# Optimization experiments

Hardware: AMD Instinct MI355X
Metric: run time of the kernel (lower is better)

The kernel has to match this reference:

```python
import jax, jax.numpy as jnp
import numpy as np
from jax import lax

B, D = 512, 256
C = 10  # hidden conv channels


def setup_inputs() -> dict:
    key = jax.random.key(0)
    ks = jax.random.split(key, 9)
    x = jax.random.normal(ks[0], (B, D, D), jnp.float32)
    w1 = jax.random.normal(ks[1], (C, 1, 1, 1), jnp.float32) * 0.1   # Conv2d(1,10,1)
    b1 = jax.random.normal(ks[2], (C,), jnp.float32) * 0.01
    w2 = jax.random.normal(ks[3], (1, C, 3, 3), jnp.float32) * 0.05  # Conv2d(10,1,3,1,1)
    b2 = jax.random.normal(ks[4], (1,), jnp.float32) * 0.01
    fc1_w = jax.random.normal(ks[5], (4, D * B), jnp.float32) * (1.0 / np.sqrt(D * B))
    fc1_b = jax.random.normal(ks[6], (4,), jnp.float32) * 0.01
    fc2_w = jax.random.normal(ks[7], (2, 4), jnp.float32) * 0.5
    fc2_b = jax.random.normal(ks[8], (2,), jnp.float32) * 0.01
    return {"x": x, "w1": w1, "b1": b1, "w2": w2, "b2": b2,
            "fc1_w": fc1_w, "fc1_b": fc1_b, "fc2_w": fc2_w, "fc2_b": fc2_b}


def reference(x, w1, b1, w2, b2, fc1_w, fc1_b, fc2_w, fc2_b):
    # edge-to-edge: E[b,i,j] = row_sum(i) + col_sum(j)
    rs = x.sum(axis=-1)          # [B, D]
    cs = x.sum(axis=-2)          # [B, D]
    e = (rs[:, :, None] + cs[:, None, :])[:, None]  # [B, 1, D, D]
    # Conv2d(1, C, 1) == per-pixel scale+bias over channels
    h = jax.nn.relu(e * w1.reshape(1, C, 1, 1) + b1.reshape(1, C, 1, 1))  # [B, C, D, D]
    # convSym: lower-triangular mask each channel
    h = h * jnp.tril(jnp.ones((D, D), jnp.float32))
    # Conv2d(C, 1, 3, stride=1, pad=1)
    y = lax.conv_general_dilated(h, w2, (1, 1), 'SAME',
                                 dimension_numbers=('NCHW', 'OIHW', 'NCHW'))
    y = jax.nn.relu(y + b2.reshape(1, 1, 1, 1))[:, 0]  # [B, D, D]
    # edge-to-vertex: v[b,i] = row_sum + col_sum
    v = y.sum(axis=-1) + y.sum(axis=-2)  # [B, D]
    flat = v.reshape(-1)                  # [B*D]
    hfc = jax.nn.relu(fc1_w @ flat + fc1_b)
    return fc2_w @ hfc + fc2_b            # [2]
```

## Files before the change

### kernel.cpp

```cpp
#include <hip/hip_runtime.h>

#define DD 256
#define BB 512
#define NL 2048

#define OFF_RS   0
#define OFF_CSP  131072
#define OFF_HFC  655360
#define OFF_PAR  655368
#define OFF_TABP 655376
#define OFF_LUT  655648

typedef float v2f __attribute__((ext_vector_type(2)));

__device__ __forceinline__ v2f mk2(float a, float b) { v2f r; r.x = a; r.y = b; return r; }

__device__ __forceinline__ v2f fma2(v2f a, v2f b, v2f c) {
#if __has_builtin(__builtin_elementwise_fma)
  return __builtin_elementwise_fma(a, b, c);
#else
  return mk2(fmaf(a.x, b.x, c.x), fmaf(a.y, b.y, c.y));
#endif
}

__device__ __forceinline__ float wave_red(float v) {
#pragma unroll
  for (int off = 32; off > 0; off >>= 1) v += __shfl_down(v, off, 64);
  return v;
}

__global__ __launch_bounds__(256) void sum_kernel(const float* __restrict__ x,
                                                  const float* __restrict__ w1,
                                                  const float* __restrict__ b1,
                                                  const float* __restrict__ w2,
                                                  float* __restrict__ ws) {
  const int bq = blockIdx.x;
  const int tid = threadIdx.x;
  if (bq == 2048) {
    const int t = tid;
    float w1v[10], b1v[10], bp[10];
    int rank[10];
#pragma unroll
    for (int c = 0; c < 10; ++c) { w1v[c] = w1[c]; b1v[c] = b1[c]; bp[c] = -b1v[c] / w1v[c]; }
#pragma unroll
    for (int c = 0; c < 10; ++c) {
      int r = 0;
#pragma unroll
      for (int k = 0; k < 10; ++k)
        r += (bp[k] < bp[c] || (bp[k] == bp[c] && k < c)) ? 1 : 0;
      rank[c] = r;
    }
    float lo = bp[0], hi = bp[0];
#pragma unroll
    for (int c = 1; c < 10; ++c) { lo = fminf(lo, bp[c]); hi = fmaxf(hi, bp[c]); }
    const float step = (hi - lo) / (float)(NL - 3);
    if (t == 0) {
      ws[OFF_PAR]     = (float)(NL - 3) / (hi - lo);
      ws[OFF_PAR + 1] = 1.0f - lo * ((float)(NL - 3) / (hi - lo));
    }
    if (t < 99) {
      const int s = t / 9, tt = t % 9;
      const int dr = tt / 3, kc = tt % 3;
      float A = 0.f, Bv = 0.f;
      for (int c = 0; c < 10; ++c) {
        bool act = (w1v[c] > 0.f) ? (rank[c] < s)
                 : ((w1v[c] < 0.f) ? (rank[c] >= s) : (b1v[c] > 0.f));
        if (act) { A += w1v[c] * w2[c * 9 + tt]; Bv += b1v[c] * w2[c * 9 + tt]; }
      }
      const int base = (s * 3 + kc) * 8;
      const int posA = (dr == 2) ? 4 : dr;
      const int posB = (dr == 2) ? 5 : (2 + dr);
      ws[OFF_TABP + base + posA] = A;
      ws[OFF_TABP + base + posB] = Bv;
      ws[OFF_TABP + base + 6] = 0.f;
      ws[OFF_TABP + base + 7] = 0.f;
    }
    unsigned short* lut = (unsigned short*)(ws + OFF_LUT);
    for (int k = t; k < NL; k += 256) {
      const float xx = lo + (float)(k - 1) * step;
      int s = 0;
#pragma unroll
      for (int c = 0; c < 10; ++c) s += (bp[c] < xx) ? 1 : 0;
      lut[k] = (unsigned short)(s * 96);
    }
    return;
  }
  const int b = bq >> 2;
  const int q = bq & 3;
  const int lane = tid & 63;
  const int wv = tid >> 6;
  __shared__ float rowp[64][65];
  __shared__ float csl[4][DD];
  __shared__ float segp[4][64];
  float4 cacc = make_float4(0.f, 0.f, 0.f, 0.f);
  const float4* px = (const float4*)(x + ((size_t)b << 16) + ((size_t)(q * 64 + wv * 16) << 8));
#pragma unroll
  for (int r = 0; r < 16; ++r) {
    float4 val = px[r * 64 + lane];
    cacc.x += val.x; cacc.y += val.y; cacc.z += val.z; cacc.w += val.w;
    rowp[wv * 16 + r][lane] = (val.x + val.y) + (val.z + val.w);
  }
  ((float4*)csl[wv])[lane] = cacc;
  __syncthreads();
  {
    const int row = tid & 63, seg = tid >> 6;
    const float* rp = rowp[row] + seg * 16;
    float s = 0.f;
#pragma unroll
    for (int k = 0; k < 16; ++k) s += rp[k];
    segp[seg][row] = s;
  }
  __syncthreads();
  if (tid < 64)
    ws[OFF_RS + b * DD + q * 64 + tid] =
        (segp[0][tid] + segp[1][tid]) + (segp[2][tid] + segp[3][tid]);
  ws[OFF_CSP + bq * DD + tid] =
      (csl[0][tid] + csl[1][tid]) + (csl[2][tid] + csl[3][tid]);
  if (bq == 0 && tid < 4) ws[OFF_HFC + tid] = 0.f;
}

__global__ __launch_bounds__(1024, 8) void conv_kernel(const float* __restrict__ b2p,
                                                       const float* __restrict__ fc1w,
                                                       float* __restrict__ ws) {
  const int b = blockIdx.x;
  const int tid = threadIdx.x;
  const int w = tid >> 6;
  const int lane = tid & 63;
  const int seg = w >> 2;
  const int wb = (w - seg) & 3;
  const int j = wb * 64 + lane;
  const int jmin = wb * 64;
  const int r0 = seg * 64, r1 = r0 + 64;

  __shared__ __align__(16) float tabP[264];
  __shared__ float rs_s[DD];
  __shared__ float cs_s[DD];
  __shared__ __align__(16) float wkA[DD][4];
  __shared__ unsigned short lut_s[NL];
  __shared__ float segsum_s[4][4];
  __shared__ float red_s[64];

  ((unsigned int*)lut_s)[tid] = ((const unsigned int*)(ws + OFF_LUT))[tid];
  if (tid < 256) {
    rs_s[tid] = ws[OFF_RS + b * DD + tid];
  } else if (tid < 512) {
    const int t = tid - 256;
    const float* csp = ws + OFF_CSP + (b * 4) * DD + t;
    cs_s[t] = (csp[0] + csp[DD]) + (csp[2 * DD] + csp[3 * DD]);
  } else if (tid < 768) {
    const int r = tid - 512;
#pragma unroll
    for (int k = 0; k < 4; ++k) wkA[r][k] = fc1w[k * (BB * DD) + b * DD + r];
  } else {
    const int u = tid - 768;
    if (u < 256) tabP[u] = ws[OFF_TABP + u];
  }
  if (tid < 8) tabP[256 + tid] = ws[OFF_TABP + 256 + tid];
  __syncthreads();
  if (tid < 16) {
    const int ss = tid >> 2, k = tid & 3;
    float s = 0.f;
#pragma unroll
    for (int r = 0; r < 64; ++r) s += wkA[ss * 64 + r][k];
    segsum_s[ss][k] = s;
  }
  __syncthreads();

  const float inv_step = ws[OFF_PAR];
  const float bias = ws[OFF_PAR + 1];
  const float b2v = b2p[0];
  const float yb = fmaxf(b2v, 0.f);
  const float fxmax = (float)(NL - 1);

  float csr[3], vf[3];
  csr[0] = (j >= 1) ? cs_s[j - 1] : 0.f;
  csr[1] = cs_s[j];
  csr[2] = (j < DD - 1) ? cs_s[j + 1] : 0.f;
  vf[0] = (j >= 1) ? 1.f : 0.f;
  vf[1] = 1.f;
  vf[2] = (j < DD - 1) ? 1.f : 0.f;
  v2f vf2[3];
#pragma unroll
  for (int kc = 0; kc < 3; ++kc) vf2[kc] = mk2(vf[kc], vf[kc]);

  const int nt = min(max(jmin - 2 - r0, 0), 64);
  const int rfirst = r0 + nt;
  const int iend = (r1 == DD) ? DD - 1 : r1;

  float P = 0.f, Q = 0.f;
  float vcol = 64.f * yb;
  v2f a01 = mk2(yb * segsum_s[seg][0], yb * segsum_s[seg][1]);
  v2f a23 = mk2(yb * segsum_s[seg][2], yb * segsum_s[seg][3]);

#define TAP_CORE(KC, E, M2, MS)                                              \
  {                                                                          \
    float fx = fmaf((E), inv_step, bias);                                    \
    fx = fminf(fmaxf(fx, 0.f), fxmax);                                       \
    const int off = (int)lut_s[(int)fx];                                     \
    const char* tp = (const char*)tabP + (off + (KC) * 32);                  \
    const float4 ab = *(const float4*)tp;                   \
    const float2 ab2 = *(const float2*)(tp + 16);                 \
    v2f tv = fma2(mk2(ab.x, ab.y), mk2((E), (E)), mk2(ab.z, ab.w));          \
    R01 = fma2((M2), tv, R01);                                               \
    R2 = fmaf((MS), fmaf(ab2.x, (E), ab2.y), R2);                            \
  }

  if (rfirst < r1) {
    if (seg > wb) {
      for (int i = r0 - 1; i <= r0; ++i) {
        const float rsv = rs_s[i];
        v2f R01 = mk2(0.f, 0.f); float R2 = 0.f;
#pragma unroll
        for (int kc = 0; kc < 3; ++kc) {
          const float e = rsv + csr[kc];
          const float m = ((j - 1 + kc) <= i) ? vf[kc] : 0.f;
          TAP_CORE(kc, e, mk2(m, m), m)
        }
        P = Q + R01.y; Q = R01.x;
      }
      for (int i = r0 + 1; i <= iend; ++i) {
        const float rsv = rs_s[i];
        v2f R01 = mk2(0.f, 0.f); float R2 = 0.f;
#pragma unroll
        for (int kc = 0; kc < 3; ++kc) {
          const float e = rsv + csr[kc];
          TAP_CORE(kc, e, vf2[kc], vf[kc])
        }
        const float yd = fmaxf(P + R2 + b2v, 0.f) - yb;
        vcol += yd;
        const float4 wkv = *(const float4*)wkA[i - 1];
        a01 = fma2(mk2(yd, yd), mk2(wkv.x, wkv.y), a01);
        a23 = fma2(mk2(yd, yd), mk2(wkv.z, wkv.w), a23);
        P = Q + R01.y; Q = R01.x;
      }
    } else {
      const int ibeg = (nt > 0) ? rfirst - 1 : ((r0 == 0) ? 0 : r0 - 1);
      const int ffrom = rfirst + 1;
      for (int i = ibeg; i <= iend; ++i) {
        const float rsv = rs_s[i];
        v2f R01 = mk2(0.f, 0.f); float R2 = 0.f;
        if (j - 1 <= i) {
#pragma unroll
          for (int kc = 0; kc < 3; ++kc) {
            const float e = rsv + csr[kc];
            const float m = ((j - 1 + kc) <= i) ? vf[kc] : 0.f;
            TAP_CORE(kc, e, mk2(m, m), m)
          }
        }
        if (i >= ffrom) {
          const float yd = fmaxf(P + R2 + b2v, 0.f) - yb;
          vcol += yd;
          const float4 wkv = *(const float4*)wkA[i - 1];
          a01 = fma2(mk2(yd, yd), mk2(wkv.x, wkv.y), a01);
          a23 = fma2(mk2(yd, yd), mk2(wkv.z, wkv.w), a23);
        }
        P = Q + R01.y; Q = R01.x;
      }
    }
  }
  if (r1 == DD) {
    const float yd = fmaxf(P + b2v, 0.f) - yb;
    vcol += yd;
    const float4 wkv = *(const float4*)wkA[DD - 1];
    a01 = fma2(mk2(yd, yd), mk2(wkv.x, wkv.y), a01);
    a23 = fma2(mk2(yd, yd), mk2(wkv.z, wkv.w), a23);
  }

  const float4 wkj = *(const float4*)wkA[j];
  a01 = fma2(mk2(vcol, vcol), mk2(wkj.x, wkj.y), a01);
  a23 = fma2(mk2(vcol, vcol), mk2(wkj.z, wkj.w), a23);

  float acc0 = wave_red(a01.x), acc1 = wave_red(a01.y);
  float acc2 = wave_red(a23.x), acc3 = wave_red(a23.y);
  if (lane == 0) {
    red_s[w * 4 + 0] = acc0; red_s[w * 4 + 1] = acc1;
    red_s[w * 4 + 2] = acc2; red_s[w * 4 + 3] = acc3;
  }
  __syncthreads();
  if (tid < 4) {
    float s = 0.f;
#pragma unroll
    for (int wv = 0; wv < 16; ++wv) s += red_s[wv * 4 + tid];
    atomicAdd(&ws[OFF_HFC + tid], s);
  }
#undef TAP_CORE
}

__global__ void fc_kernel(const float* __restrict__ fc1b, const float* __restrict__ fc2w,
                          const float* __restrict__ fc2b, const float* __restrict__ ws,
                          float* __restrict__ out) {
  if (threadIdx.x == 0 && blockIdx.x == 0) {
    float o0 = fc2b[0], o1 = fc2b[1];
#pragma unroll
    for (int k = 0; k < 4; ++k) {
      float h = fmaxf(ws[OFF_HFC + k] + fc1b[k], 0.f);
      o0 += fc2w[k] * h;
      o1 += fc2w[4 + k] * h;
    }
    out[0] = o0; out[1] = o1;
  }
}

extern "C" void kernel_launch(void* const* d_in, const int* in_sizes, int n_in,
                              void* d_out, int out_size, void* d_ws, size_t ws_size,
                              hipStream_t stream) {
  const float* x    = (const float*)d_in[0];
  const float* w1   = (const float*)d_in[1];
  const float* b1   = (const float*)d_in[2];
  const float* w2   = (const float*)d_in[3];
  const float* b2   = (const float*)d_in[4];
  const float* fc1w = (const float*)d_in[5];
  const float* fc1b = (const float*)d_in[6];
  const float* fc2w = (const float*)d_in[7];
  const float* fc2b = (const float*)d_in[8];
  float* out = (float*)d_out;
  float* ws  = (float*)d_ws;

  hipLaunchKernelGGL(sum_kernel,  dim3(2049), dim3(256), 0, stream, x, w1, b1, w2, ws);
  hipLaunchKernelGGL(conv_kernel, dim3(512), dim3(1024), 0, stream, b2, fc1w, ws);
  hipLaunchKernelGGL(fc_kernel,   dim3(1), dim3(64), 0, stream, fc1b, fc2w, fc2b, ws, out);
}
```

Baseline: 241.6 us.

## Fuse sum and conv kernels into one per-batch kernel with LDS-staged loads

Merges the row/column-sum pass and the conv/FC pass into a single kernel with one block per batch. Each block streams its 256x256 slice into LDS with double-buffered global_load_lds and computes row sums via wave reductions. Each block also recomputes the breakpoint tables and LUT locally instead of reading them from a workspace. Per-block FC partials go to the workspace and a 256-thread final kernel reduces them, replacing the global atomics. This removes a launch and the workspace round-trip, but the x read now runs with only 512 blocks of 1024 threads and less parallelism per batch.

Result: slower. 255.8 us (+5.9%).

```diff
diff --git a/kernel.cpp b/kernel.cpp
--- a/kernel.cpp
+++ b/kernel.cpp
@@ -4,12 +4,7 @@
 #define BB 512
 #define NL 2048
 
-#define OFF_RS   0
-#define OFF_CSP  131072
-#define OFF_HFC  655360
-#define OFF_PAR  655368
-#define OFF_TABP 655376
-#define OFF_LUT  655648
+#define OFF_PART 0
 
 typedef float v2f __attribute__((ext_vector_type(2)));
 
@@ -29,39 +24,62 @@
   return v;
 }
 
-__global__ __launch_bounds__(256) void sum_kernel(const float* __restrict__ x,
-                                                  const float* __restrict__ w1,
-                                                  const float* __restrict__ b1,
-                                                  const float* __restrict__ w2,
-                                                  float* __restrict__ ws) {
-  const int bq = blockIdx.x;
+__device__ __forceinline__ void glds16(const float* src, float* lds_dst) {
+  __builtin_amdgcn_global_load_lds(
+      (const __attribute__((address_space(1))) unsigned int*)src,
+      (__attribute__((address_space(3))) unsigned int*)lds_dst, 16, 0, 0);
+}
+
+__global__ __launch_bounds__(1024, 4) void fused_kernel(
+    const float* __restrict__ x, const float* __restrict__ w1,
+    const float* __restrict__ b1, const float* __restrict__ w2,
+    const float* __restrict__ b2p, const float* __restrict__ fc1w,
+    float* __restrict__ ws) {
+  const int b = blockIdx.x;
   const int tid = threadIdx.x;
-  if (bq == 2048) {
-    const int t = tid;
+  const int w = tid >> 6;
+  const int lane = tid & 63;
+
+  __shared__ __align__(16) float stage[16 * 2 * DD];
+  __shared__ __align__(16) float tabP[264];
+  __shared__ float rs_s[DD];
+  __shared__ float cs_s[DD];
+  __shared__ __align__(16) float wkA[DD][4];
+  __shared__ unsigned short lut_s[NL];
+  __shared__ __align__(16) float csl[16][DD];
+  __shared__ float segsum_s[4][4];
+  __shared__ float red_s[64];
+
+  float wk0 = 0.f, wk1 = 0.f, wk2 = 0.f, wk3 = 0.f;
+  if (tid < 256) {
+    wk0 = fc1w[0 * (BB * DD) + b * DD + tid];
+    wk1 = fc1w[1 * (BB * DD) + b * DD + tid];
+    wk2 = fc1w[2 * (BB * DD) + b * DD + tid];
+    wk3 = fc1w[3 * (BB * DD) + b * DD + tid];
+  }
+
+  {
     float w1v[10], b1v[10], bp[10];
-    int rank[10];
 #pragma unroll
     for (int c = 0; c < 10; ++c) { w1v[c] = w1[c]; b1v[c] = b1[c]; bp[c] = -b1v[c] / w1v[c]; }
-#pragma unroll
-    for (int c = 0; c < 10; ++c) {
-      int r = 0;
-#pragma unroll
-      for (int k = 0; k < 10; ++k)
-        r += (bp[k] < bp[c] || (bp[k] == bp[c] && k < c)) ? 1 : 0;
-      rank[c] = r;
-    }
     float lo = bp[0], hi = bp[0];
 #pragma unroll
     for (int c = 1; c < 10; ++c) { lo = fminf(lo, bp[c]); hi = fmaxf(hi, bp[c]); }
     const float step = (hi - lo) / (float)(NL - 3);
-    if (t == 0) {
-      ws[OFF_PAR]     = (float)(NL - 3) / (hi - lo);
-      ws[OFF_PAR + 1] = 1.0f - lo * ((float)(NL - 3) / (hi - lo));
-    }
-    if (t < 99) {
-      const int s = t / 9, tt = t % 9;
+    if (tid < 99) {
+      int rank[10];
+#pragma unroll
+      for (int c = 0; c < 10; ++c) {
+        int r = 0;
+#pragma unroll
+        for (int k = 0; k < 10; ++k)
+          r += (bp[k] < bp[c] || (bp[k] == bp[c] && k < c)) ? 1 : 0;
+        rank[c] = r;
+      }
+      const int s = tid / 9, tt = tid % 9;
       const int dr = tt / 3, kc = tt % 3;
       float A = 0.f, Bv = 0.f;
+#pragma unroll
       for (int c = 0; c < 10; ++c) {
         bool act = (w1v[c] > 0.f) ? (rank[c] < s)
                  : ((w1v[c] < 0.f) ? (rank[c] >= s) : (b1v[c] > 0.f));
@@ -70,104 +88,78 @@
       const int base = (s * 3 + kc) * 8;
       const int posA = (dr == 2) ? 4 : dr;
       const int posB = (dr == 2) ? 5 : (2 + dr);
-      ws[OFF_TABP + base + posA] = A;
-      ws[OFF_TABP + base + posB] = Bv;
-      ws[OFF_TABP + base + 6] = 0.f;
-      ws[OFF_TABP + base + 7] = 0.f;
-    }
-    unsigned short* lut = (unsigned short*)(ws + OFF_LUT);
-    for (int k = t; k < NL; k += 256) {
+      tabP[base + posA] = A;
+      tabP[base + posB] = Bv;
+      tabP[base + 6] = 0.f;
+      tabP[base + 7] = 0.f;
+    }
+    for (int k = tid; k < NL; k += 1024) {
       const float xx = lo + (float)(k - 1) * step;
       int s = 0;
 #pragma unroll
       for (int c = 0; c < 10; ++c) s += (bp[c] < xx) ? 1 : 0;
-      lut[k] = (unsigned short)(s * 96);
-    }
-    return;
-  }
-  const int b = bq >> 2;
-  const int q = bq & 3;
-  const int lane = tid & 63;
-  const int wv = tid >> 6;
-  __shared__ float rowp[64][65];
-  __shared__ float csl[4][DD];
-  __shared__ float segp[4][64];
-  float4 cacc = make_float4(0.f, 0.f, 0.f, 0.f);
-  const float4* px = (const float4*)(x + ((size_t)b << 16) + ((size_t)(q * 64 + wv * 16) << 8));
-#pragma unroll
-  for (int r = 0; r < 16; ++r) {
-    float4 val = px[r * 64 + lane];
-    cacc.x += val.x; cacc.y += val.y; cacc.z += val.z; cacc.w += val.w;
-    rowp[wv * 16 + r][lane] = (val.x + val.y) + (val.z + val.w);
-  }
-  ((float4*)csl[wv])[lane] = cacc;
+      lut_s[k] = (unsigned short)(s * 96);
+    }
+  }
+
+  {
+    float* mystage = &stage[w * (2 * DD)];
+    const float* gx = x + ((size_t)b << 16) + (size_t)(w * 16) * DD;
+    glds16(gx + 0 * DD + lane * 4, mystage + 0);
+    glds16(gx + 1 * DD + lane * 4, mystage + DD);
+    float4 cacc = make_float4(0.f, 0.f, 0.f, 0.f);
+#pragma unroll
+    for (int r = 0; r < 16; ++r) {
+      if (r < 15) asm volatile("s_waitcnt vmcnt(1)" ::: "memory");
+      else        asm volatile("s_waitcnt vmcnt(0)" ::: "memory");
+      __builtin_amdgcn_sched_barrier(0);
+      const float4 v = ((const float4*)(mystage + (r & 1) * DD))[lane];
+      cacc.x += v.x; cacc.y += v.y; cacc.z += v.z; cacc.w += v.w;
+      float rsum = (v.x + v.y) + (v.z + v.w);
+      __builtin_amdgcn_sched_barrier(0);
+      if (r + 2 < 16)
+        glds16(gx + (r + 2) * DD + lane * 4, mystage + (r & 1) * DD);
+      rsum = wave_red(rsum);
+      if (lane == 0) rs_s[w * 16 + r] = rsum;
+    }
+    ((float4*)csl[w])[lane] = cacc;
+    if (tid < 256) { wkA[tid][0] = wk0; wkA[tid][1] = wk1; wkA[tid][2] = wk2; wkA[tid][3] = wk3; }
+  }
   __syncthreads();
-  {
-    const int row = tid & 63, seg = tid >> 6;
-    const float* rp = rowp[row] + seg * 16;
+  if (tid < 256) {
+    float s0 = 0.f;
+#pragma unroll
+    for (int q = 0; q < 16; ++q) s0 += csl[q][tid];
+    cs_s[tid] = s0;
+  } else if (tid < 272) {
+    const int t = tid - 256;
+    const int ss = t >> 2, k = t & 3;
     float s = 0.f;
 #pragma unroll
-    for (int k = 0; k < 16; ++k) s += rp[k];
-    segp[seg][row] = s;
+    for (int r = 0; r < 64; ++r) s += wkA[ss * 64 + r][k];
+    segsum_s[ss][k] = s;
   }
   __syncthreads();
-  if (tid < 64)
-    ws[OFF_RS + b * DD + q * 64 + tid] =
-        (segp[0][tid] + segp[1][tid]) + (segp[2][tid] + segp[3][tid]);
-  ws[OFF_CSP + bq * DD + tid] =
-      (csl[0][tid] + csl[1][tid]) + (csl[2][tid] + csl[3][tid]);
-  if (bq == 0 && tid < 4) ws[OFF_HFC + tid] = 0.f;
-}
-
-__global__ __launch_bounds__(1024, 8) void conv_kernel(const float* __restrict__ b2p,
-                                                       const float* __restrict__ fc1w,
-                                                       float* __restrict__ ws) {
-  const int b = blockIdx.x;
-  const int tid = threadIdx.x;
-  const int w = tid >> 6;
-  const int lane = tid & 63;
+
   const int seg = w >> 2;
   const int wb = (w - seg) & 3;
   const int j = wb * 64 + lane;
   const int jmin = wb * 64;
   const int r0 = seg * 64, r1 = r0 + 64;
 
-  __shared__ __align__(16) float tabP[264];
-  __shared__ float rs_s[DD];
-  __shared__ float cs_s[DD];
-  __shared__ __align__(16) float wkA[DD][4];
-  __shared__ unsigned short lut_s[NL];
-  __shared__ float segsum_s[4][4];
-  __shared__ float red_s[64];
-
-  ((unsigned int*)lut_s)[tid] = ((const unsigned int*)(ws + OFF_LUT))[tid];
-  if (tid < 256) {
-    rs_s[tid] = ws[OFF_RS + b * DD + tid];
-  } else if (tid < 512) {
-    const int t = tid - 256;
-    const float* csp = ws + OFF_CSP + (b * 4) * DD + t;
-    cs_s[t] = (csp[0] + csp[DD]) + (csp[2 * DD] + csp[3 * DD]);
-  } else if (tid < 768) {
-    const int r = tid - 512;
-#pragma unroll
-    for (int k = 0; k < 4; ++k) wkA[r][k] = fc1w[k * (BB * DD) + b * DD + r];
-  } else {
-    const int u = tid - 768;
-    if (u < 256) tabP[u] = ws[OFF_TABP + u];
-  }
-  if (tid < 8) tabP[256 + tid] = ws[OFF_TABP + 256 + tid];
-  __syncthreads();
-  if (tid < 16) {
-    const int ss = tid >> 2, k = tid & 3;
-    float s = 0.f;
-#pragma unroll
-    for (int r = 0; r < 64; ++r) s += wkA[ss * 64 + r][k];
-    segsum_s[ss][k] = s;
-  }
-  __syncthreads();
-
-  const float inv_step = ws[OFF_PAR];
-  const float bias = ws[OFF_PAR + 1];
+  const float inv_step_c = [] __device__ () { return 0.f; }();
+  (void)inv_step_c;
+  float lo_c, hi_c;
+  {
+    float bp0[10];
+#pragma unroll
+    for (int c = 0; c < 10; ++c) bp0[c] = -b1[c] / w1[c];
+    lo_c = bp0[0]; hi_c = bp0[0];
+#pragma unroll
+    for (int c = 1; c < 10; ++c) { lo_c = fminf(lo_c, bp0[c]); hi_c = fmaxf(hi_c, bp0[c]); }
+  }
+  const float inv_step = (float)(NL - 3) / (hi_c - lo_c);
+  const float bias = 1.0f - lo_c * inv_step;
   const float b2v = b2p[0];
   const float yb = fmaxf(b2v, 0.f);
   const float fxmax = (float)(NL - 1);
@@ -281,7 +273,7 @@
     float s = 0.f;
 #pragma unroll
     for (int wv = 0; wv < 16; ++wv) s += red_s[wv * 4 + tid];
-    atomicAdd(&ws[OFF_HFC + tid], s);
+    ws[OFF_PART + b * 4 + tid] = s;
   }
 #undef TAP_CORE
 }
@@ -289,13 +281,22 @@
 __global__ void fc_kernel(const float* __restrict__ fc1b, const float* __restrict__ fc2w,
                           const float* __restrict__ fc2b, const float* __restrict__ ws,
                           float* __restrict__ out) {
-  if (threadIdx.x == 0 && blockIdx.x == 0) {
+  const int tid = threadIdx.x;
+  const int k = tid >> 6, lane = tid & 63;
+  __shared__ float hfc_s[4];
+  float s = 0.f;
+#pragma unroll
+  for (int m = 0; m < 8; ++m) s += ws[OFF_PART + (lane + m * 64) * 4 + k];
+  s = wave_red(s);
+  if (lane == 0) hfc_s[k] = s;
+  __syncthreads();
+  if (tid == 0) {
     float o0 = fc2b[0], o1 = fc2b[1];
 #pragma unroll
-    for (int k = 0; k < 4; ++k) {
-      float h = fmaxf(ws[OFF_HFC + k] + fc1b[k], 0.f);
-      o0 += fc2w[k] * h;
-      o1 += fc2w[4 + k] * h;
+    for (int kk = 0; kk < 4; ++kk) {
+      float h = fmaxf(hfc_s[kk] + fc1b[kk], 0.f);
+      o0 += fc2w[kk] * h;
+      o1 += fc2w[4 + kk] * h;
     }
     out[0] = o0; out[1] = o1;
   }
@@ -316,7 +317,8 @@
   float* out = (float*)d_out;
   float* ws  = (float*)d_ws;
 
-  hipLaunchKernelGGL(sum_kernel,  dim3(2049), dim3(256), 0, stream, x, w1, b1, w2, ws);
-  hipLaunchKernelGGL(conv_kernel, dim3(512), dim3(1024), 0, stream, b2, fc1w, ws);
-  hipLaunchKernelGGL(fc_kernel,   dim3(1), dim3(64), 0, stream, fc1b, fc2w, fc2b, ws, out);
-}
+  hipLaunchKernelGGL(fused_kernel, dim3(512), dim3(1024), 0, stream,
+                     x, w1, b1, w2, b2, fc1w, ws);
+  hipLaunchKernelGGL(fc_kernel, dim3(1), dim3(256), 0, stream,
+                     fc1b, fc2w, fc2b, ws, out);
+}
```

## Rebalance conv waves over lower-triangular rows with per-wave row ranges

Applied to the files above, without the earlier changes.

Replaces the fixed 4x4 grid of 64-row segments per column block with a hand-tuned table that assigns each of the 16 waves a column block and a row range covering only the lower-triangular region. Waves that previously had no work above the diagonal are reassigned, so the triangular workload is spread more evenly and the slowest wave finishes sooner. The diagonal-crossing loop is split into a masked part up to the block's last column and an unmasked tail. The constant yb contribution that was seeded per wave is moved into a single per-block correction before the atomic add. The partitioning is hardcoded for D=256.

Result: no change. 239.7 us (-0.8%).

```diff
diff --git a/kernel.cpp b/kernel.cpp
--- a/kernel.cpp
+++ b/kernel.cpp
@@ -126,11 +126,28 @@
   const int tid = threadIdx.x;
   const int w = tid >> 6;
   const int lane = tid & 63;
-  const int seg = w >> 2;
-  const int wb = (w - seg) & 3;
-  const int j = wb * 64 + lane;
+
+  int wb, r0, r1;
+  switch (w) {
+    case 0:  wb = 0; r0 = 0;   r1 = 43;  break;
+    case 1:  wb = 0; r0 = 43;  r1 = 86;  break;
+    case 2:  wb = 0; r0 = 86;  r1 = 129; break;
+    case 3:  wb = 0; r0 = 129; r1 = 172; break;
+    case 4:  wb = 0; r0 = 172; r1 = 214; break;
+    case 5:  wb = 0; r0 = 214; r1 = 256; break;
+    case 6:  wb = 1; r0 = 62;  r1 = 101; break;
+    case 7:  wb = 1; r0 = 101; r1 = 140; break;
+    case 8:  wb = 1; r0 = 140; r1 = 179; break;
+    case 9:  wb = 1; r0 = 179; r1 = 218; break;
+    case 10: wb = 1; r0 = 218; r1 = 256; break;
+    case 11: wb = 2; r0 = 126; r1 = 170; break;
+    case 12: wb = 2; r0 = 170; r1 = 213; break;
+    case 13: wb = 2; r0 = 213; r1 = 256; break;
+    case 14: wb = 3; r0 = 190; r1 = 223; break;
+    default: wb = 3; r0 = 223; r1 = 256; break;
+  }
   const int jmin = wb * 64;
-  const int r0 = seg * 64, r1 = r0 + 64;
+  const int j = jmin + lane;
 
   __shared__ __align__(16) float tabP[264];
   __shared__ float rs_s[DD];
@@ -183,14 +200,13 @@
 #pragma unroll
   for (int kc = 0; kc < 3; ++kc) vf2[kc] = mk2(vf[kc], vf[kc]);
 
-  const int nt = min(max(jmin - 2 - r0, 0), 64);
-  const int rfirst = r0 + nt;
+  const int dlim = jmin + 63;
   const int iend = (r1 == DD) ? DD - 1 : r1;
 
   float P = 0.f, Q = 0.f;
-  float vcol = 64.f * yb;
-  v2f a01 = mk2(yb * segsum_s[seg][0], yb * segsum_s[seg][1]);
-  v2f a23 = mk2(yb * segsum_s[seg][2], yb * segsum_s[seg][3]);
+  float vcol = 0.f;
+  v2f a01 = mk2(0.f, 0.f);
+  v2f a23 = mk2(0.f, 0.f);
 
 #define TAP_CORE(KC, E, M2, MS)                                              \
   {                                                                          \
@@ -205,57 +221,72 @@
     R2 = fmaf((MS), fmaf(ab2.x, (E), ab2.y), R2);                            \
   }
 
-  if (rfirst < r1) {
-    if (seg > wb) {
-      for (int i = r0 - 1; i <= r0; ++i) {
-        const float rsv = rs_s[i];
-        v2f R01 = mk2(0.f, 0.f); float R2 = 0.f;
+  if (r0 >= dlim) {
+    for (int i = r0 - 1; i <= r0; ++i) {
+      const float rsv = rs_s[i];
+      v2f R01 = mk2(0.f, 0.f); float R2 = 0.f;
+#pragma unroll
+      for (int kc = 0; kc < 3; ++kc) {
+        const float e = rsv + csr[kc];
+        const float m = ((j - 1 + kc) <= i) ? vf[kc] : 0.f;
+        TAP_CORE(kc, e, mk2(m, m), m)
+      }
+      (void)R2;
+      P = Q + R01.y; Q = R01.x;
+    }
+    for (int i = r0 + 1; i <= iend; ++i) {
+      const float rsv = rs_s[i];
+      v2f R01 = mk2(0.f, 0.f); float R2 = 0.f;
+#pragma unroll
+      for (int kc = 0; kc < 3; ++kc) {
+        const float e = rsv + csr[kc];
+        TAP_CORE(kc, e, vf2[kc], vf[kc])
+      }
+      const float yd = fmaxf(P + R2 + b2v, 0.f) - yb;
+      vcol += yd;
+      const float4 wkv = *(const float4*)wkA[i - 1];
+      a01 = fma2(mk2(yd, yd), mk2(wkv.x, wkv.y), a01);
+      a23 = fma2(mk2(yd, yd), mk2(wkv.z, wkv.w), a23);
+      P = Q + R01.y; Q = R01.x;
+    }
+  } else {
+    const int ibeg = (r0 == 0) ? 0 : r0 - 1;
+    const int ffrom = r0 + 1;
+    const int gend = (iend < dlim) ? iend : dlim;
+    for (int i = ibeg; i <= gend; ++i) {
+      const float rsv = rs_s[i];
+      v2f R01 = mk2(0.f, 0.f); float R2 = 0.f;
+      if (j - 1 <= i) {
 #pragma unroll
         for (int kc = 0; kc < 3; ++kc) {
           const float e = rsv + csr[kc];
           const float m = ((j - 1 + kc) <= i) ? vf[kc] : 0.f;
           TAP_CORE(kc, e, mk2(m, m), m)
         }
-        P = Q + R01.y; Q = R01.x;
-      }
-      for (int i = r0 + 1; i <= iend; ++i) {
-        const float rsv = rs_s[i];
-        v2f R01 = mk2(0.f, 0.f); float R2 = 0.f;
-#pragma unroll
-        for (int kc = 0; kc < 3; ++kc) {
-          const float e = rsv + csr[kc];
-          TAP_CORE(kc, e, vf2[kc], vf[kc])
-        }
+      }
+      if (i >= ffrom) {
         const float yd = fmaxf(P + R2 + b2v, 0.f) - yb;
         vcol += yd;
         const float4 wkv = *(const float4*)wkA[i - 1];
         a01 = fma2(mk2(yd, yd), mk2(wkv.x, wkv.y), a01);
         a23 = fma2(mk2(yd, yd), mk2(wkv.z, wkv.w), a23);
-        P = Q + R01.y; Q = R01.x;
-      }
-    } else {
-      const int ibeg = (nt > 0) ? rfirst - 1 : ((r0 == 0) ? 0 : r0 - 1);
-      const int ffrom = rfirst + 1;
-      for (int i = ibeg; i <= iend; ++i) {
-        const float rsv = rs_s[i];
-        v2f R01 = mk2(0.f, 0.f); float R2 = 0.f;
-        if (j - 1 <= i) {
-#pragma unroll
-          for (int kc = 0; kc < 3; ++kc) {
-            const float e = rsv + csr[kc];
-            const float m = ((j - 1 + kc) <= i) ? vf[kc] : 0.f;
-            TAP_CORE(kc, e, mk2(m, m), m)
-          }
-        }
-        if (i >= ffrom) {
-          const float yd = fmaxf(P + R2 + b2v, 0.f) - yb;
-          vcol += yd;
-          const float4 wkv = *(const float4*)wkA[i - 1];
-          a01 = fma2(mk2(yd, yd), mk2(wkv.x, wkv.y), a01);
-          a23 = fma2(mk2(yd, yd), mk2(wkv.z, wkv.w), a23);
-        }
-        P = Q + R01.y; Q = R01.x;
-      }
+      }
+      P = Q + R01.y; Q = R01.x;
+    }
+    for (int i = dlim + 1; i <= iend; ++i) {
+      const float rsv = rs_s[i];
+      v2f R01 = mk2(0.f, 0.f); float R2 = 0.f;
+#pragma unroll
+      for (int kc = 0; kc < 3; ++kc) {
+        const float e = rsv + csr[kc];
+        TAP_CORE(kc, e, vf2[kc], vf[kc])
+      }
+      const float yd = fmaxf(P + R2 + b2v, 0.f) - yb;
+      vcol += yd;
+      const float4 wkv = *(const float4*)wkA[i - 1];
+      a01 = fma2(mk2(yd, yd), mk2(wkv.x, wkv.y), a01);
+      a23 = fma2(mk2(yd, yd), mk2(wkv.z, wkv.w), a23);
+      P = Q + R01.y; Q = R01.x;
     }
   }
   if (r1 == DD) {
@@ -281,6 +312,9 @@
     float s = 0.f;
 #pragma unroll
     for (int wv = 0; wv < 16; ++wv) s += red_s[wv * 4 + tid];
+    const float wt = (segsum_s[0][tid] + segsum_s[1][tid]) +
+                     (segsum_s[2][tid] + segsum_s[3][tid]);
+    s = fmaf(512.f * yb, wt, s);
     atomicAdd(&ws[OFF_HFC + tid], s);
   }
 #undef TAP_CORE
```
